# Performance work log

Hardware: AMD Instinct MI355X
Metric: run time of the kernel (lower is better)

The kernel has to match this reference:

```python
import jax, jax.numpy as jnp
import numpy as np

H = 2048   # hidden_size
NH = 32    # n_head
HS = 64    # head_size
B, T = 2, 4096
D_DECAY, D_AAA, D_MV, D_GATE = 96, 96, 64, 256


def setup_inputs() -> dict:
    key = jax.random.key(0)
    ks = jax.random.split(key, 30)
    rn = lambda k, s, sc=0.02: jax.random.normal(k, s, jnp.float32) * sc
    d = {}
    d['x'] = jax.random.normal(ks[0], (B, T, H), jnp.float32)
    d['shift_state_in'] = jax.random.normal(ks[1], (B, H), jnp.float32)
    d['wkv_state_in'] = jnp.zeros((B, NH, HS, HS), jnp.float32)
    d['v_first_val'] = jax.random.normal(ks[2], (B, T, H), jnp.float32)
    for i, n in enumerate(['x_r', 'x_w', 'x_k', 'x_v', 'x_a', 'x_g']):
        d[n] = jax.random.uniform(ks[3 + i], (H,), jnp.float32)
    d['w0'] = rn(ks[9], (H,)) - 4.0
    d['w1'] = rn(ks[10], (H, D_DECAY)); d['w2'] = rn(ks[11], (D_DECAY, H))
    d['a0'] = rn(ks[12], (H,)); d['a1'] = rn(ks[13], (H, D_AAA)); d['a2'] = rn(ks[14], (D_AAA, H))
    d['v0'] = rn(ks[15], (H,)) + 1.0; d['v1'] = rn(ks[16], (H, D_MV)); d['v2'] = rn(ks[17], (D_MV, H))
    d['g1'] = rn(ks[18], (H, D_GATE)); d['g2'] = rn(ks[19], (D_GATE, H))
    d['k_k'] = jnp.full((H,), 0.85, jnp.float32)
    d['k_a'] = jnp.ones((H,), jnp.float32)
    d['r_k'] = rn(ks[20], (NH, HS))
    s = 1.0 / np.sqrt(H)
    d['W_r'] = jax.random.normal(ks[21], (H, H), jnp.float32) * s
    d['W_k'] = jax.random.normal(ks[22], (H, H), jnp.float32) * s
    d['W_v'] = jax.random.normal(ks[23], (H, H), jnp.float32) * s
    d['W_o'] = jax.random.normal(ks[24], (H, H), jnp.float32) * s
    d['ln_w'] = jnp.ones((H,), jnp.float32)
    d['ln_b'] = jnp.zeros((H,), jnp.float32)
    return d


def _forward(x, shift_state_in, wkv_state_in, v_first_val, x_r, x_w, x_k, x_v, x_a, x_g,
             w0, w1, w2, a0, a1, a2, v0, v1, v2, g1, g2, k_k, k_a, r_k,
             W_r, W_k, W_v, W_o, ln_w, ln_b):
    Bx, Tx, C = x.shape
    # token shift: previous token embedding (shift_state for t=0)
    xprev = jnp.concatenate([shift_state_in[:, None, :], x[:, :-1]], axis=1)
    dx = xprev - x
    xr, xw, xk, xv, xa, xg = (x + dx * m for m in (x_r, x_w, x_k, x_v, x_a, x_g))
    r = xr @ W_r.T
    k = xk @ W_k.T
    v = xv @ W_v.T
    # soft-clamped log-decay (<= -0.5)
    w_raw = -jax.nn.softplus(-(w0 + jnp.tanh(xw @ w1) @ w2)) - 0.5
    # layer_id > 0: residual mix with first-layer value
    v = v + (v_first_val - v) * jax.nn.sigmoid(v0 + (xv @ v1) @ v2)
    a = jax.nn.sigmoid(a0 + (xa @ a1) @ a2)          # in-context learning rate
    g = jax.nn.sigmoid(xg @ g1) @ g2                 # output gate
    kk = (k * k_k).reshape(Bx, Tx, NH, HS)
    kk = kk / jnp.maximum(jnp.linalg.norm(kk, axis=-1, keepdims=True), 1e-12)  # F.normalize
    kk = kk.reshape(Bx, Tx, C)
    k = k * (1.0 + (a - 1.0) * k_a)
    w = jnp.exp(-jnp.exp(w_raw))                     # per-channel decay in (0,1)
    heads = lambda t: t.reshape(Bx, Tx, NH, HS).transpose(1, 0, 2, 3)  # [T,B,NH,HS]
    rs, ws, ks_, vs, kks, as_ = map(heads, (r, w, k, v, kk, a))

    def step(S, inp):
        # S: [B,NH,HS(value),HS(key)]
        rt, wt, kt, vt, kkt, at = inp
        sa = jnp.einsum('bhvk,bhk->bhv', S, -kkt)
        S = (S * wt[:, :, None, :]
             + sa[:, :, :, None] * (kkt * at)[:, :, None, :]
             + vt[:, :, :, None] * kt[:, :, None, :])
        return S, jnp.einsum('bhvk,bhk->bhv', S, rt)

    wkv_state_out, y = jax.lax.scan(step, wkv_state_in, (rs, ws, ks_, vs, kks, as_))
    y = y.transpose(1, 0, 2, 3)                      # [B,T,NH,HS]
    # GroupNorm(n_head groups, eps=1e-5*head_size)
    mu = y.mean(-1, keepdims=True)
    var = y.var(-1, keepdims=True)
    y = ((y - mu) / jnp.sqrt(var + 1e-5 * HS)).reshape(Bx, Tx, C) * ln_w + ln_b
    rk = (r.reshape(Bx, Tx, NH, HS) * k.reshape(Bx, Tx, NH, HS) * r_k).sum(-1, keepdims=True)
    y = y + (rk * v.reshape(Bx, Tx, NH, HS)).reshape(Bx, Tx, C)
    out = (y * g) @ W_o.T
    return out, x[:, -1], wkv_state_out, v_first_val


def reference(x, shift_state_in, wkv_state_in, v_first_val, x_r, x_w, x_k, x_v, x_a, x_g,
              w0, w1, w2, a0, a1, a2, v0, v1, v2, g1, g2, k_k, k_a, r_k,
              W_r, W_k, W_v, W_o, ln_w, ln_b):
    return _forward(x, shift_state_in, wkv_state_in, v_first_val, x_r, x_w, x_k, x_v, x_a, x_g,
                    w0, w1, w2, a0, a1, a2, v0, v1, v2, g1, g2, k_k, k_a, r_k,
                    W_r, W_k, W_v, W_o, ln_w, ln_b)
```

## Files before the change

kernel.cpp:

```cpp
#include <hip/hip_runtime.h>

typedef unsigned short u16;
typedef __attribute__((ext_vector_type(4))) float f32x4;
typedef __attribute__((ext_vector_type(8))) __bf16 bf16x8;
typedef __attribute__((ext_vector_type(8))) unsigned short u16x8;
typedef __attribute__((ext_vector_type(4))) unsigned short u16x4;

#define DI static __device__ __forceinline__

DI float bfu2f(u16 u){ unsigned int x = ((unsigned int)u)<<16; float f; __builtin_memcpy(&f,&x,4); return f; }
DI u16 f2bfu(float f){ __bf16 h = (__bf16)f; u16 u; __builtin_memcpy(&u,&h,2); return u; }
DI float sigm(float x){ return 1.f/(1.f+expf(-x)); }

DI void gload_lds16(const void* g, void* l) {
  __builtin_amdgcn_global_load_lds(
      (const __attribute__((address_space(1))) unsigned int*)g,
      (__attribute__((address_space(3))) unsigned int*)l, 16, 0, 0);
}

template<bool OBF16>
__global__ __launch_bounds__(256) void gemm128_k(
    const u16* __restrict__ A, const u16* __restrict__ Bt,
    void* __restrict__ Cp, int M, int N, int K)
{
  __shared__ alignas(16) u16 As[128*64];
  __shared__ alignas(16) u16 Bs[128*64];
  const int tid = threadIdx.x;
  const int wid = tid >> 6, lane = tid & 63;
  const int wm = wid >> 1, wn = wid & 1;
  const int l15 = lane & 15, q = lane >> 4;
  const int m0 = blockIdx.x * 128, n0 = blockIdx.y * 128;
  const int sr = (wid << 3) + (lane >> 3);
  const int sc = (lane & 7) << 3;
  f32x4 acc[4][4];
  #pragma unroll
  for (int i=0;i<4;i++)
    #pragma unroll
    for (int j=0;j<4;j++) acc[i][j] = f32x4{0.f,0.f,0.f,0.f};

  char* la = (char*)As + (size_t)wid*1024;
  char* lb = (char*)Bs + (size_t)wid*1024;
  for (int k0 = 0; k0 < K; k0 += 64) {
    const u16* ga = A  + (size_t)(m0 + sr)*K + k0 + sc;
    const u16* gb = Bt + (size_t)(n0 + sr)*K + k0 + sc;
    #pragma unroll
    for (int it = 0; it < 4; ++it) {
      gload_lds16(ga + (size_t)(32*it)*K, la + it*4096);
      gload_lds16(gb + (size_t)(32*it)*K, lb + it*4096);
    }
    __syncthreads();
    #pragma unroll
    for (int ks = 0; ks < 64; ks += 32) {
      bf16x8 af[4], bfv[4];
      #pragma unroll
      for (int i=0;i<4;i++) af[i]  = *(const bf16x8*)&As[(wm*64 + i*16 + l15)*64 + ks + q*8];
      #pragma unroll
      for (int j=0;j<4;j++) bfv[j] = *(const bf16x8*)&Bs[(wn*64 + j*16 + l15)*64 + ks + q*8];
      #pragma unroll
      for (int i=0;i<4;i++)
        #pragma unroll
        for (int j=0;j<4;j++)
          acc[i][j] = __builtin_amdgcn_mfma_f32_16x16x32_bf16(af[i], bfv[j], acc[i][j], 0, 0, 0);
    }
    __syncthreads();
  }
  #pragma unroll
  for (int i=0;i<4;i++)
    #pragma unroll
    for (int j=0;j<4;j++)
      #pragma unroll
      for (int rr=0;rr<4;rr++) {
        const int gm = m0 + wm*64 + i*16 + q*4 + rr;
        const int gn = n0 + wn*64 + j*16 + l15;
        const size_t o = (size_t)gm * (size_t)N + gn;
        if constexpr (OBF16) ((u16*)Cp)[o] = f2bfu(acc[i][j][rr]);
        else                 ((float*)Cp)[o] = acc[i][j][rr];
      }
}

constexpr int LDW = 72;

template<bool MIX, bool WNK, bool ABF16, bool OBF16, int EPI=0>
__global__ __launch_bounds__(256) void gemm_k(
    const void* __restrict__ Ap, const float* __restrict__ dxp, const float* __restrict__ mixp,
    const float* __restrict__ Wp, void* __restrict__ Cp, int M, int N, int K)
{
  __shared__ alignas(16) __bf16 As[64*LDW];
  __shared__ alignas(16) __bf16 Bs[64*LDW];
  const int tid = threadIdx.x;
  const int m0 = blockIdx.x * 64;
  const int n0 = blockIdx.y * 64;
  const int lane = tid & 63, wid = tid >> 6;
  const int wm = wid >> 1, wn = wid & 1;
  const int l15 = lane & 15, q = lane >> 4;
  f32x4 acc[2][2] = {{{0.f,0.f,0.f,0.f},{0.f,0.f,0.f,0.f}},
                     {{0.f,0.f,0.f,0.f},{0.f,0.f,0.f,0.f}}};

  for (int k0 = 0; k0 < K; k0 += 64) {
    {
      const int kc = (tid & 7) * 8;
      const int r0 = tid >> 3;
      #pragma unroll
      for (int it = 0; it < 2; ++it) {
        const int row = r0 + 32*it;
        const size_t gmK = (size_t)(m0 + row) * (size_t)K;
        const int gk = k0 + kc;
        if constexpr (ABF16) {
          const u16* A16 = (const u16*)Ap;
          u16x8 u;
          if (gk + 7 < K) u = *(const u16x8*)(A16 + gmK + gk);
          else {
            #pragma unroll
            for (int e=0;e<8;e++) u[e] = (gk+e < K) ? A16[gmK + gk + e] : (u16)0;
          }
          *(u16x8*)&As[row*LDW + kc] = u;
        } else {
          const float* A32 = (const float*)Ap;
          float f[8];
          if (gk + 7 < K) {
            f32x4 va = *(const f32x4*)(A32 + gmK + gk);
            f32x4 vb = *(const f32x4*)(A32 + gmK + gk + 4);
            if constexpr (MIX) {
              f32x4 d0 = *(const f32x4*)(dxp + gmK + gk);
              f32x4 d1 = *(const f32x4*)(dxp + gmK + gk + 4);
              f32x4 c0 = *(const f32x4*)(mixp + gk);
              f32x4 c1 = *(const f32x4*)(mixp + gk + 4);
              va = va + d0*c0; vb = vb + d1*c1;
            }
            #pragma unroll
            for (int e=0;e<4;e++){ f[e]=va[e]; f[4+e]=vb[e]; }
          } else {
            #pragma unroll
            for (int e=0;e<8;e++){
              const int kk2 = gk+e;
              float xv = 0.f;
              if (kk2 < K) {
                xv = A32[gmK + kk2];
                if constexpr (MIX) xv = fmaf(dxp[gmK+kk2], mixp[kk2], xv);
              }
              f[e] = xv;
            }
          }
          bf16x8 v8;
          #pragma unroll
          for (int e=0;e<8;e++) v8[e] = (__bf16)f[e];
          *(bf16x8*)&As[row*LDW + kc] = v8;
        }
      }
    }
    if constexpr (WNK) {
      const int kc = (tid & 7) * 8;
      const int r0 = tid >> 3;
      #pragma unroll
      for (int it = 0; it < 2; ++it) {
        const int row = r0 + 32*it;
        const int gn = n0 + row;
        const int gk = k0 + kc;
        float f[8];
        if (gn < N && gk + 7 < K) {
          const size_t o = (size_t)gn * (size_t)K + gk;
          f32x4 va = *(const f32x4*)(Wp + o);
          f32x4 vb = *(const f32x4*)(Wp + o + 4);
          #pragma unroll
          for (int e=0;e<4;e++){ f[e]=va[e]; f[4+e]=vb[e]; }
        } else {
          #pragma unroll
          for (int e=0;e<8;e++) f[e] = (gn < N && gk+e < K) ? Wp[(size_t)gn*K + gk + e] : 0.f;
        }
        bf16x8 v8;
        #pragma unroll
        for (int e=0;e<8;e++) v8[e] = (__bf16)f[e];
        *(bf16x8*)&Bs[row*LDW + kc] = v8;
      }
    } else {
      const int nc = (tid & 15) * 4;
      const int kr = tid >> 4;
      #pragma unroll
      for (int it = 0; it < 4; ++it) {
        const int kk = kr + 16*it;
        const int gk = k0 + kk;
        f32x4 v = {0.f,0.f,0.f,0.f};
        if (gk < K) {
          const int gn = n0 + nc;
          if (gn + 3 < N) v = *(const f32x4*)(Wp + (size_t)gk*N + gn);
          else {
            #pragma unroll
            for (int e=0;e<4;e++) if (gn+e < N) v[e] = Wp[(size_t)gk*N + gn + e];
          }
        }
        #pragma unroll
        for (int e=0;e<4;e++) Bs[(nc+e)*LDW + kk] = (__bf16)v[e];
      }
    }
    __syncthreads();
    #pragma unroll
    for (int ks = 0; ks < 64; ks += 32) {
      bf16x8 af[2], bfv[2];
      #pragma unroll
      for (int i=0;i<2;i++) af[i]  = *(const bf16x8*)&As[(wm*32 + i*16 + l15)*LDW + ks + q*8];
      #pragma unroll
      for (int i=0;i<2;i++) bfv[i] = *(const bf16x8*)&Bs[(wn*32 + i*16 + l15)*LDW + ks + q*8];
      #pragma unroll
      for (int i=0;i<2;i++)
        #pragma unroll
        for (int j=0;j<2;j++)
          acc[i][j] = __builtin_amdgcn_mfma_f32_16x16x32_bf16(af[i], bfv[j], acc[i][j], 0, 0, 0);
    }
    __syncthreads();
  }
  #pragma unroll
  for (int i=0;i<2;i++) {
    #pragma unroll
    for (int j=0;j<2;j++) {
      #pragma unroll
      for (int rr=0;rr<4;rr++) {
        const int gm = m0 + wm*32 + i*16 + q*4 + rr;
        const int gn = n0 + wn*32 + j*16 + l15;
        if (gn < N) {
          const size_t o = (size_t)gm * (size_t)N + gn;
          if constexpr (EPI == 1) {
            float* C = (float*)Cp;
            const float s = sigm(mixp[gn] + acc[i][j][rr]);
            const float vG = C[o];
            C[o] = vG + (dxp[o] - vG) * s;
          } else if constexpr (OBF16) {
            ((u16*)Cp)[o] = f2bfu(acc[i][j][rr]);
          } else {
            ((float*)Cp)[o] = acc[i][j][rr];
          }
        }
      }
    }
  }
}

__global__ void mix_cast_k(const float* __restrict__ x, const float* __restrict__ shift,
    const float* __restrict__ mr, const float* __restrict__ mw, const float* __restrict__ mk,
    const float* __restrict__ mv, const float* __restrict__ ma, const float* __restrict__ mg,
    u16* __restrict__ xr_b, u16* __restrict__ xw_b, u16* __restrict__ xk_b,
    u16* __restrict__ xv_b, u16* __restrict__ xa_b, u16* __restrict__ xg_b,
    float* __restrict__ xlast, int T_, int B_)
{
  const int Hh = 2048;
  size_t e4 = (size_t)blockIdx.x*blockDim.x + threadIdx.x;
  size_t total4 = (size_t)B_*T_*Hh/4;
  if (e4 >= total4) return;
  size_t e = e4*4;
  size_t th = (size_t)T_*Hh;
  size_t b = e / th; size_t rem = e - b*th;
  int t = (int)(rem / Hh); int c = (int)(rem & (Hh-1));
  f32x4 xv4 = *(const f32x4*)(x+e);
  f32x4 xp = t ? *(const f32x4*)(x+e-Hh) : *(const f32x4*)(shift + b*Hh + c);
  f32x4 dx = xp - xv4;
  if (t == T_-1) *(f32x4*)(xlast + b*Hh + c) = xv4;
  #define EMIT(mp, dst) { \
    f32x4 mc = *(const f32x4*)(mp + c); \
    f32x4 r_ = xv4 + dx*mc; \
    u16x4 o_; \
    o_[0]=f2bfu(r_[0]); o_[1]=f2bfu(r_[1]); o_[2]=f2bfu(r_[2]); o_[3]=f2bfu(r_[3]); \
    *(u16x4*)(dst + e) = o_; }
  EMIT(mr, xr_b) EMIT(mw, xw_b) EMIT(mk, xk_b)
  EMIT(mv, xv_b) EMIT(ma, xa_b) EMIT(mg, xg_b)
  #undef EMIT
}

__global__ void castw_k(const float* __restrict__ src, u16* __restrict__ dst, long n4){
  long i = (long)blockIdx.x*blockDim.x + threadIdx.x;
  if (i < n4) {
    f32x4 v = ((const f32x4*)src)[i];
    u16x4 o; o[0]=f2bfu(v[0]); o[1]=f2bfu(v[1]); o[2]=f2bfu(v[2]); o[3]=f2bfu(v[3]);
    ((u16x4*)dst)[i] = o;
  }
}

__global__ void ew_tanh_k(u16* p, long n){
  long i = (long)blockIdx.x*blockDim.x + threadIdx.x;
  if (i < n) p[i] = f2bfu(tanhf(bfu2f(p[i])));
}
__global__ void ew_sig_k(u16* p, long n){
  long i = (long)blockIdx.x*blockDim.x + threadIdx.x;
  if (i < n) p[i] = f2bfu(sigm(bfu2f(p[i])));
}
__global__ void ew_w_k(float* p, const float* __restrict__ w0, long n){
  long i = (long)blockIdx.x*blockDim.x + threadIdx.x;
  if (i < n) {
    int c = (int)(i & 2047);
    float z = -(w0[c] + p[i]);
    float sp = (z > 20.f) ? z : log1pf(expf(z));
    p[i] = expf(-expf(-sp - 0.5f));
  }
}
__global__ void ew_a_k(u16* p, const float* __restrict__ a0, long n){
  long i = (long)blockIdx.x*blockDim.x + threadIdx.x;
  if (i < n) { int c = (int)(i & 2047); p[i] = f2bfu(sigm(a0[c] + bfu2f(p[i]))); }
}
__global__ void copy4_k(float* __restrict__ dst, const float* __restrict__ src, long n4){
  long i = (long)blockIdx.x*blockDim.x + threadIdx.x;
  if (i < n4) ((f32x4*)dst)[i] = ((const f32x4*)src)[i];
}

__global__ __launch_bounds__(256) void rnorm_k(
    const u16* __restrict__ kb, const float* __restrict__ kkw, float* __restrict__ r2)
{
  const size_t bt = blockIdx.x;
  const int tid = threadIdx.x;
  const int c0 = tid << 3;
  u16x8 kv8 = *(const u16x8*)(kb + bt*2048 + c0);
  f32x4 ka_ = *(const f32x4*)(kkw + c0);
  f32x4 kb_ = *(const f32x4*)(kkw + c0 + 4);
  float s = 0.f;
  #pragma unroll
  for (int e=0;e<4;e++){ float kk = bfu2f(kv8[e])*ka_[e];   s = fmaf(kk,kk,s); }
  #pragma unroll
  for (int e=0;e<4;e++){ float kk = bfu2f(kv8[4+e])*kb_[e]; s = fmaf(kk,kk,s); }
  s += __shfl_xor(s, 1, 64);
  s += __shfl_xor(s, 2, 64);
  s += __shfl_xor(s, 4, 64);
  if ((tid & 7) == 0) r2[bt*32 + (tid>>3)] = 1.f/fmaxf(s, 1e-24f);
}

__global__ __launch_bounds__(64) __attribute__((amdgpu_waves_per_eu(1, 4)))
void scan_k(
    const u16* __restrict__ rb, const float* __restrict__ wb, const u16* __restrict__ kb,
    const float* __restrict__ vb, const u16* __restrict__ ab,
    const float* __restrict__ kkw, const float* __restrict__ kaw,
    const float* __restrict__ S0, float* __restrict__ yb, float* __restrict__ Sout, int T_)
{
  const int Hh = 2048, NHl = 32;
  const int blk = blockIdx.x;
  const int b = blk >> 5, h = blk & 31;
  const int lane = threadIdx.x;
  float S[64];
  const size_t sbase = (((size_t)b*NHl + h)*64 + lane)*64;
  #pragma unroll
  for (int i=0;i<64;i++) S[i] = S0[sbase+i];
  const float kkc = kkw[h*64+lane], kac = kaw[h*64+lane];
  __shared__ alignas(16) float lw[64], lkk[64], lka[64], lke[64], lr[64];
  size_t idx = (size_t)b*T_*Hh + (size_t)h*64 + lane;
  float rv = bfu2f(rb[idx]), wv = wb[idx], kv = bfu2f(kb[idx]), vv = vb[idx], av = bfu2f(ab[idx]);
  for (int t=0; t<T_; ++t) {
    float kk = kv * kkc;
    float ssum = kk*kk;
    #pragma unroll
    for (int m=1;m<64;m<<=1) ssum += __shfl_xor(ssum, m, 64);
    float inv = 1.f / fmaxf(sqrtf(ssum), 1e-12f);
    float kkn = kk * inv;
    float ke  = kv * (1.f + (av - 1.f)*kac);
    lw[lane]=wv; lkk[lane]=kkn; lka[lane]=kkn*av; lke[lane]=ke; lr[lane]=rv;
    const float vt = vv;
    __syncthreads();
    float nrv=0.f,nwv=0.f,nkv=0.f,nvv=0.f,nav=0.f;
    if (t+1 < T_) {
      const size_t ni = idx + Hh;
      nrv = bfu2f(rb[ni]); nwv = wb[ni]; nkv = bfu2f(kb[ni]); nvv = vb[ni]; nav = bfu2f(ab[ni]);
    }
    const f32x4* KK4 = (const f32x4*)lkk;
    const f32x4* W4  = (const f32x4*)lw;
    const f32x4* KA4 = (const f32x4*)lka;
    const f32x4* KE4 = (const f32x4*)lke;
    const f32x4* R4  = (const f32x4*)lr;
    float sa0=0.f,sa1=0.f,sa2=0.f,sa3=0.f;
    #pragma unroll
    for (int qq=0;qq<16;qq++){
      f32x4 k4 = KK4[qq];
      sa0 = fmaf(S[4*qq+0], k4[0], sa0);
      sa1 = fmaf(S[4*qq+1], k4[1], sa1);
      sa2 = fmaf(S[4*qq+2], k4[2], sa2);
      sa3 = fmaf(S[4*qq+3], k4[3], sa3);
    }
    const float sa = -((sa0+sa1)+(sa2+sa3));
    float y0=0.f,y1=0.f,y2=0.f,y3=0.f;
    #pragma unroll
    for (int qq=0;qq<16;qq++){
      f32x4 w4=W4[qq], a4=KA4[qq], e4=KE4[qq], r4=R4[qq];
      float s_;
      s_ = fmaf(vt, e4[0], fmaf(sa, a4[0], S[4*qq+0]*w4[0])); S[4*qq+0]=s_; y0 = fmaf(s_, r4[0], y0);
      s_ = fmaf(vt, e4[1], fmaf(sa, a4[1], S[4*qq+1]*w4[1])); S[4*qq+1]=s_; y1 = fmaf(s_, r4[1], y1);
      s_ = fmaf(vt, e4[2], fmaf(sa, a4[2], S[4*qq+2]*w4[2])); S[4*qq+2]=s_; y2 = fmaf(s_, r4[2], y2);
      s_ = fmaf(vt, e4[3], fmaf(sa, a4[3], S[4*qq+3]*w4[3])); S[4*qq+3]=s_; y3 = fmaf(s_, r4[3], y3);
    }
    yb[idx] = (y0+y1)+(y2+y3);
    __syncthreads();
    rv=nrv; wv=nwv; kv=nkv; vv=nvv; av=nav;
    idx += Hh;
  }
  #pragma unroll
  for (int i=0;i<64;i++) Sout[sbase+i] = S[i];
}

__global__ __launch_bounds__(64) void chunk_mu_k(
    const float* __restrict__ wb, const u16* __restrict__ kb,
    const float* __restrict__ vb, const u16* __restrict__ ab,
    const float* __restrict__ kkw, const float* __restrict__ kaw,
    const float* __restrict__ r2b,
    float* __restrict__ Mbuf, float* __restrict__ Ubuf, int T_, int NC)
{
  const int bid = blockIdx.x;
  const int ch  = bid >> 1;
  const bool idrow = ((bid & 1) == 0);
  const int c  = ch % NC;
  const int bh = ch / NC;
  const int b = bh >> 5, h = bh & 31;
  const int lane = threadIdx.x;

  float S[64];
  #pragma unroll
  for (int i=0;i<64;i++) S[i] = (idrow && lane == i) ? 1.f : 0.f;

  const int hc = h*64 + lane;
  const float kkc = kkw[hc], kac = kaw[hc];

  __shared__ alignas(16) float LB[2][4][64];

  size_t idx = ((size_t)b*T_ + (size_t)c*64)*2048 + hc;
  size_t r2i = ((size_t)b*T_ + (size_t)c*64)*32 + h;

  {
    const float kv = bfu2f(kb[idx]);
    const float av = bfu2f(ab[idx]);
    const float kk = kv*kkc;
    LB[0][0][lane] = wb[idx];
    LB[0][1][lane] = kk;
    LB[0][2][lane] = kk*av;
    if (!idrow) LB[0][3][lane] = kv*(1.f+(av-1.f)*kac);
  }
  float vv = idrow ? 0.f : vb[idx];
  float r2 = r2b[r2i];
  __syncthreads();

  for (int j=0; j<64; ++j) {
    const int cur = j & 1;
    float nk=0.f,nw=0.f,na=0.f,nv=0.f,nr2=0.f;
    if (j+1 < 64) {
      const size_t ni = idx + 2048;
      nk = bfu2f(kb[ni]); nw = wb[ni]; na = bfu2f(ab[ni]);
      if (!idrow) nv = vb[ni];
      nr2 = r2b[r2i + 32];
    }
    const f32x4* W4  = (const f32x4*)LB[cur][0];
    const f32x4* KK4 = (const f32x4*)LB[cur][1];
    const f32x4* KA4 = (const f32x4*)LB[cur][2];
    const f32x4* KE4 = (const f32x4*)LB[cur][3];
    float sa0=0.f,sa1=0.f,sa2=0.f,sa3=0.f;
    #pragma unroll
    for (int qq=0;qq<16;qq++){
      f32x4 k4 = KK4[qq];
      sa0 = fmaf(S[4*qq+0], k4[0], sa0);
      sa1 = fmaf(S[4*qq+1], k4[1], sa1);
      sa2 = fmaf(S[4*qq+2], k4[2], sa2);
      sa3 = fmaf(S[4*qq+3], k4[3], sa3);
    }
    const float sa = -((sa0+sa1)+(sa2+sa3)) * r2;
    const float vtv = vv;
    if (idrow) {
      #pragma unroll
      for (int qq=0;qq<16;qq++){
        f32x4 w4=W4[qq], a4=KA4[qq];
        S[4*qq+0] = fmaf(sa, a4[0], S[4*qq+0]*w4[0]);
        S[4*qq+1] = fmaf(sa, a4[1], S[4*qq+1]*w4[1]);
        S[4*qq+2] = fmaf(sa, a4[2], S[4*qq+2]*w4[2]);
        S[4*qq+3] = fmaf(sa, a4[3], S[4*qq+3]*w4[3]);
      }
    } else {
      #pragma unroll
      for (int qq=0;qq<16;qq++){
        f32x4 w4=W4[qq], a4=KA4[qq], e4=KE4[qq];
        S[4*qq+0] = fmaf(vtv, e4[0], fmaf(sa, a4[0], S[4*qq+0]*w4[0]));
        S[4*qq+1] = fmaf(vtv, e4[1], fmaf(sa, a4[1], S[4*qq+1]*w4[1]));
        S[4*qq+2] = fmaf(vtv, e4[2], fmaf(sa, a4[2], S[4*qq+2]*w4[2]));
        S[4*qq+3] = fmaf(vtv, e4[3], fmaf(sa, a4[3], S[4*qq+3]*w4[3]));
      }
    }
    if (j+1 < 64) {
      const float kk = nk*kkc;
      LB[cur^1][0][lane] = nw;
      LB[cur^1][1][lane] = kk;
      LB[cur^1][2][lane] = kk*na;
      if (!idrow) LB[cur^1][3][lane] = nk*(1.f+(na-1.f)*kac);
    }
    __syncthreads();
    vv = nv; r2 = nr2;
    idx += 2048; r2i += 32;
  }
  float* dst = (idrow ? Mbuf : Ubuf) + (size_t)ch*4096 + (size_t)lane*64;
  #pragma unroll
  for (int qq=0;qq<16;qq++)
    *(f32x4*)(dst + 4*qq) = f32x4{S[4*qq+0],S[4*qq+1],S[4*qq+2],S[4*qq+3]};
}

__global__ __launch_bounds__(256) void propagate_k(
    const float* __restrict__ Mbuf, const float* __restrict__ Ubuf,
    const float* __restrict__ S0, float* __restrict__ SSbuf, float* __restrict__ Sout, int NC)
{
  const int bh   = blockIdx.x >> 2;
  const int v0r  = (blockIdx.x & 3) * 16;
  const int tid  = threadIdx.x;
  const int lane = tid & 63;
  const int wvv  = tid >> 6;

  __shared__ float MT[64*65];
  __shared__ float Srow[16][64];

  #pragma unroll
  for (int i=0;i<4;i++) {
    const int v = v0r + wvv*4 + i;
    Srow[wvv*4+i][lane] = S0[((size_t)bh*64 + v)*64 + lane];
  }

  const size_t mbase = (size_t)bh * NC * 4096;
  f32x4 mreg[4];
  #pragma unroll
  for (int it=0; it<4; ++it)
    mreg[it] = *(const f32x4*)(Mbuf + mbase + it*1024 + tid*4);

  for (int c=0; c<NC; ++c) {
    const size_t chB = mbase + (size_t)c*4096;
    #pragma unroll
    for (int it=0; it<4; ++it) {
      const int base = it*1024 + tid*4;
      const int j = base >> 6;
      const int k = base & 63;
      #pragma unroll
      for (int e=0;e<4;e++) MT[(k+e)*65 + j] = mreg[it][e];
    }
    __syncthreads();
    if (c+1 < NC) {
      #pragma unroll
      for (int it=0; it<4; ++it)
        mreg[it] = *(const f32x4*)(Mbuf + chB + 4096 + it*1024 + tid*4);
    }
    #pragma unroll
    for (int i=0;i<4;i++)
      SSbuf[chB + (size_t)(v0r + wvv*4 + i)*64 + lane] = Srow[wvv*4+i][lane];
    float u[4];
    #pragma unroll
    for (int i=0;i<4;i++)
      u[i] = Ubuf[chB + (size_t)(v0r + wvv*4 + i)*64 + lane];
    float acc[4] = {0.f,0.f,0.f,0.f};
    #pragma unroll
    for (int j4=0; j4<16; ++j4) {
      float m0_ = MT[lane*65 + j4*4 + 0];
      float m1_ = MT[lane*65 + j4*4 + 1];
      float m2_ = MT[lane*65 + j4*4 + 2];
      float m3_ = MT[lane*65 + j4*4 + 3];
      #pragma unroll
      for (int i=0;i<4;i++) {
        f32x4 s4 = *(const f32x4*)&Srow[wvv*4+i][j4*4];
        acc[i] = fmaf(s4[0], m0_, acc[i]);
        acc[i] = fmaf(s4[1], m1_, acc[i]);
        acc[i] = fmaf(s4[2], m2_, acc[i]);
        acc[i] = fmaf(s4[3], m3_, acc[i]);
      }
    }
    #pragma unroll
    for (int i=0;i<4;i++) Srow[wvv*4+i][lane] = acc[i] + u[i];
    __syncthreads();
  }
  #pragma unroll
  for (int i=0;i<4;i++) {
    const int v = v0r + wvv*4 + i;
    Sout[((size_t)bh*64 + v)*64 + lane] = Srow[wvv*4+i][lane];
  }
}

__global__ __launch_bounds__(64) void replay_k(
    const u16* __restrict__ rb, const float* __restrict__ wb, const u16* __restrict__ kb,
    const float* __restrict__ vb, const u16* __restrict__ ab,
    const float* __restrict__ kkw, const float* __restrict__ kaw,
    const float* __restrict__ r2b,
    const float* __restrict__ SSbuf, float* __restrict__ yb, int T_, int NC)
{
  const int ch = blockIdx.x;
  const int c  = ch % NC;
  const int bh = ch / NC;
  const int b = bh >> 5, h = bh & 31;
  const int lane = threadIdx.x;
  float S[64];
  const float* sp = SSbuf + (size_t)ch*4096 + (size_t)lane*64;
  #pragma unroll
  for (int qq=0;qq<16;qq++){
    f32x4 v4 = *(const f32x4*)(sp + 4*qq);
    S[4*qq+0]=v4[0]; S[4*qq+1]=v4[1]; S[4*qq+2]=v4[2]; S[4*qq+3]=v4[3];
  }
  const int hc = h*64 + lane;
  const float kkc = kkw[hc], kac = kaw[hc];
  __shared__ alignas(16) float LB[2][5][64];
  size_t idx = ((size_t)b*T_ + (size_t)c*64)*2048 + hc;
  size_t r2i = ((size_t)b*T_ + (size_t)c*64)*32 + h;
  {
    const float kv = bfu2f(kb[idx]);
    const float av = bfu2f(ab[idx]);
    const float kk = kv*kkc;
    LB[0][0][lane] = wb[idx];
    LB[0][1][lane] = kk;
    LB[0][2][lane] = kk*av;
    LB[0][3][lane] = kv*(1.f+(av-1.f)*kac);
    LB[0][4][lane] = bfu2f(rb[idx]);
  }
  float vv = vb[idx];
  float r2 = r2b[r2i];
  __syncthreads();

  for (int t=0; t<64; ++t) {
    const int cur = t & 1;
    float nr=0.f,nw=0.f,nk=0.f,nv=0.f,na=0.f,nr2=0.f;
    if (t+1 < 64) {
      const size_t ni = idx + 2048;
      nr = bfu2f(rb[ni]); nw = wb[ni]; nk = bfu2f(kb[ni]); nv = vb[ni]; na = bfu2f(ab[ni]);
      nr2 = r2b[r2i + 32];
    }
    const f32x4* W4  = (const f32x4*)LB[cur][0];
    const f32x4* KK4 = (const f32x4*)LB[cur][1];
    const f32x4* KA4 = (const f32x4*)LB[cur][2];
    const f32x4* KE4 = (const f32x4*)LB[cur][3];
    const f32x4* R4  = (const f32x4*)LB[cur][4];
    float sa0=0.f,sa1=0.f,sa2=0.f,sa3=0.f;
    #pragma unroll
    for (int qq=0;qq<16;qq++){
      f32x4 k4 = KK4[qq];
      sa0 = fmaf(S[4*qq+0], k4[0], sa0);
      sa1 = fmaf(S[4*qq+1], k4[1], sa1);
      sa2 = fmaf(S[4*qq+2], k4[2], sa2);
      sa3 = fmaf(S[4*qq+3], k4[3], sa3);
    }
    const float sa = -((sa0+sa1)+(sa2+sa3)) * r2;
    const float vt = vv;
    float y0=0.f,y1=0.f,y2=0.f,y3=0.f;
    #pragma unroll
    for (int qq=0;qq<16;qq++){
      f32x4 w4=W4[qq], a4=KA4[qq], e4=KE4[qq], r4=R4[qq];
      float s_;
      s_ = fmaf(vt, e4[0], fmaf(sa, a4[0], S[4*qq+0]*w4[0])); S[4*qq+0]=s_; y0 = fmaf(s_, r4[0], y0);
      s_ = fmaf(vt, e4[1], fmaf(sa, a4[1], S[4*qq+1]*w4[1])); S[4*qq+1]=s_; y1 = fmaf(s_, r4[1], y1);
      s_ = fmaf(vt, e4[2], fmaf(sa, a4[2], S[4*qq+2]*w4[2])); S[4*qq+2]=s_; y2 = fmaf(s_, r4[2], y2);
      s_ = fmaf(vt, e4[3], fmaf(sa, a4[3], S[4*qq+3]*w4[3])); S[4*qq+3]=s_; y3 = fmaf(s_, r4[3], y3);
    }
    yb[idx] = (y0+y1)+(y2+y3);
    if (t+1 < 64) {
      const float kk = nk*kkc;
      LB[cur^1][0][lane] = nw;
      LB[cur^1][1][lane] = kk;
      LB[cur^1][2][lane] = kk*na;
      LB[cur^1][3][lane] = nk*(1.f+(na-1.f)*kac);
      LB[cur^1][4][lane] = nr;
    }
    __syncthreads();
    vv = nv; r2 = nr2;
    idx += 2048; r2i += 32;
  }
}

__global__ __launch_bounds__(256) void post_k(
    const float* __restrict__ yb, const u16* __restrict__ rb, const u16* __restrict__ kb,
    const u16* __restrict__ ab, const u16* __restrict__ gb, const float* __restrict__ vb,
    const float* __restrict__ kaw, const float* __restrict__ rkw,
    const float* __restrict__ lnw, const float* __restrict__ lnb, u16* __restrict__ zb)
{
  const int wid = threadIdx.x >> 6, lane = threadIdx.x & 63;
  const size_t unit = (size_t)blockIdx.x*4 + wid;
  const size_t bt = unit >> 5; const int h = (int)(unit & 31);
  const size_t idx = bt*2048 + (size_t)h*64 + lane;
  const int hc = h*64 + lane;
  const float yv = yb[idx];
  const float rv = bfu2f(rb[idx]), kv = bfu2f(kb[idx]), av = bfu2f(ab[idx]);
  const float ke = kv*(1.f + (av-1.f)*kaw[hc]);
  float s1 = yv, s2 = yv*yv, rk = rv*ke*rkw[hc];
  #pragma unroll
  for (int m=1;m<64;m<<=1){
    s1 += __shfl_xor(s1,m,64);
    s2 += __shfl_xor(s2,m,64);
    rk += __shfl_xor(rk,m,64);
  }
  const float mean = s1 * (1.f/64.f);
  const float var  = s2 * (1.f/64.f) - mean*mean;
  const float rstd = rsqrtf(var + 6.4e-4f);
  const float zn = (yv-mean)*rstd*lnw[hc] + lnb[hc] + rk*vb[idx];
  zb[idx] = f2bfu(zn * bfu2f(gb[idx]));
}

extern "C" void kernel_launch(void* const* d_in, const int* in_sizes, int n_in,
                              void* d_out, int out_size, void* d_ws, size_t ws_size,
                              hipStream_t stream)
{
  const float* x      = (const float*)d_in[0];
  const float* shift  = (const float*)d_in[1];
  const float* wkv0   = (const float*)d_in[2];
  const float* vfirst = (const float*)d_in[3];
  const float* xr = (const float*)d_in[4];
  const float* xw = (const float*)d_in[5];
  const float* xk = (const float*)d_in[6];
  const float* xv = (const float*)d_in[7];
  const float* xa = (const float*)d_in[8];
  const float* xg = (const float*)d_in[9];
  const float* w0 = (const float*)d_in[10];
  const float* w1 = (const float*)d_in[11];
  const float* w2 = (const float*)d_in[12];
  const float* a0 = (const float*)d_in[13];
  const float* a1 = (const float*)d_in[14];
  const float* a2 = (const float*)d_in[15];
  const float* v0 = (const float*)d_in[16];
  const float* v1 = (const float*)d_in[17];
  const float* v2 = (const float*)d_in[18];
  const float* g1 = (const float*)d_in[19];
  const float* g2 = (const float*)d_in[20];
  const float* k_k = (const float*)d_in[21];
  const float* k_a = (const float*)d_in[22];
  const float* r_k = (const float*)d_in[23];
  const float* W_r = (const float*)d_in[24];
  const float* W_k = (const float*)d_in[25];
  const float* W_v = (const float*)d_in[26];
  const float* W_o = (const float*)d_in[27];
  const float* ln_w = (const float*)d_in[28];
  const float* ln_b = (const float*)d_in[29];

  const int H = 2048, NH = 32;
  const int BH = in_sizes[1];
  const int B  = BH / H;
  const long BTH = (long)in_sizes[0];
  const int T  = (int)(BTH / BH);
  const int M  = (int)(BTH / H);

  float* out0 = (float*)d_out;
  float* out1 = out0 + BTH;
  float* out2 = out1 + BH;
  float* out3 = out2 + (size_t)B*NH*64*64;

  char* ws = (char*)d_ws;
  u16* mixb = (u16*)ws;  ws += (size_t)BTH*12;
  u16* xr_b = mixb + 0*BTH;
  u16* xw_b = mixb + 1*BTH;
  u16* xk_b = mixb + 2*BTH;
  u16* xv_b = mixb + 3*BTH;
  u16* xa_b = mixb + 4*BTH;
  u16* xg_b = mixb + 5*BTH;
  float* Mbuf  = (float*)mixb;
  float* Ubuf  = Mbuf + BTH;
  float* SSbuf = Ubuf + BTH;
  u16*   zb16  = (u16*)mixb;
  u16* rb   = (u16*)ws;  ws += BTH*2;
  u16* kb   = (u16*)ws;  ws += BTH*2;
  u16* ab   = (u16*)ws;  ws += BTH*2;
  u16* gb   = (u16*)ws;  ws += BTH*2;
  u16* wr16 = (u16*)ws;  ws += (size_t)H*H*2;
  u16* wk16 = (u16*)ws;  ws += (size_t)H*H*2;
  u16* wv16 = (u16*)ws;  ws += (size_t)H*H*2;
  u16* wo16 = (u16*)ws;  ws += (size_t)H*H*2;
  u16* h1w  = (u16*)ws;  ws += (size_t)M*96*2;
  u16* h1a  = (u16*)ws;  ws += (size_t)M*96*2;
  u16* h1v  = (u16*)ws;  ws += (size_t)M*64*2;
  u16* h1g  = (u16*)ws;  ws += (size_t)M*256*2;
  float* dxz = (float*)ws; ws += BTH*4;
  float* r2b = (float*)h1w;
  const size_t ws_need = (size_t)(ws - (char*)d_ws);
  const bool chunked = (ws_size >= ws_need) && (T % 64 == 0);
  const bool big_ok  = (M % 128 == 0);
  (void)n_in; (void)out_size;

  const dim3 blk(256);
  auto gg  = [&](int N){ return dim3(M/64, (N+63)/64); };
  auto gg128 = [&](int N){ return dim3(M/128, N/128); };

  mix_cast_k<<<dim3((unsigned)((BTH/4 + 255)/256)), blk, 0, stream>>>(
      x, shift, xr, xw, xk, xv, xa, xg, xr_b, xw_b, xk_b, xv_b, xa_b, xg_b, out1, T, B);

  {
    const long n4 = (long)H*H/4;
    const dim3 gw((unsigned)((n4 + 255)/256));
    castw_k<<<gw, blk, 0, stream>>>(W_r, wr16, n4);
    castw_k<<<gw, blk, 0, stream>>>(W_k, wk16, n4);
    castw_k<<<gw, blk, 0, stream>>>(W_v, wv16, n4);
    castw_k<<<gw, blk, 0, stream>>>(W_o, wo16, n4);
  }

  gemm_k<false,false,true,true><<<gg(96),  blk, 0, stream>>>(xw_b, nullptr, nullptr, w1, h1w, M, 96,  H);
  gemm_k<false,false,true,true><<<gg(96),  blk, 0, stream>>>(xa_b, nullptr, nullptr, a1, h1a, M, 96,  H);
  gemm_k<false,false,true,true><<<gg(64),  blk, 0, stream>>>(xv_b, nullptr, nullptr, v1, h1v, M, 64,  H);
  gemm_k<false,false,true,true><<<gg(256), blk, 0, stream>>>(xg_b, nullptr, nullptr, g1, h1g, M, 256, H);

  ew_tanh_k<<<dim3((unsigned)(((long)M*96 + 255)/256)),  blk, 0, stream>>>(h1w, (long)M*96);
  ew_sig_k <<<dim3((unsigned)(((long)M*256 + 255)/256)), blk, 0, stream>>>(h1g, (long)M*256);

  if (big_ok) {
    gemm128_k<true ><<<gg128(H), blk, 0, stream>>>(xr_b, wr16, rb,   M, H, H);
    gemm128_k<true ><<<gg128(H), blk, 0, stream>>>(xk_b, wk16, kb,   M, H, H);
    gemm128_k<false><<<gg128(H), blk, 0, stream>>>(xv_b, wv16, out3, M, H, H);
  } else {
    gemm_k<false,true,true,true ><<<gg(H), blk, 0, stream>>>(xr_b, nullptr, nullptr, W_r, rb,   M, H, H);
    gemm_k<false,true,true,true ><<<gg(H), blk, 0, stream>>>(xk_b, nullptr, nullptr, W_k, kb,   M, H, H);
    gemm_k<false,true,true,false><<<gg(H), blk, 0, stream>>>(xv_b, nullptr, nullptr, W_v, out3, M, H, H);
  }

  gemm_k<false,false,true,false  ><<<gg(H), blk, 0, stream>>>(h1w, nullptr, nullptr, w2, dxz, M, H, 96);
  rnorm_k<<<dim3((unsigned)M), blk, 0, stream>>>(kb, k_k, r2b);
  gemm_k<false,false,true,true   ><<<gg(H), blk, 0, stream>>>(h1a, nullptr, nullptr, a2, ab,  M, H, 96);
  gemm_k<false,false,true,false,1><<<gg(H), blk, 0, stream>>>(h1v, vfirst,  v0,      v2, out3, M, H, 64);
  gemm_k<false,false,true,true   ><<<gg(H), blk, 0, stream>>>(h1g, nullptr, nullptr, g2, gb,  M, H, 256);

  const unsigned nbB = (unsigned)((BTH + 255)/256);
  ew_w_k<<<dim3(nbB), blk, 0, stream>>>(dxz, w0, BTH);
  ew_a_k<<<dim3(nbB), blk, 0, stream>>>(ab, a0, BTH);

  if (chunked) {
    const int NC = T / 64;
    const int CH = B * NH * NC;
    chunk_mu_k <<<dim3(2*CH),   dim3(64),  0, stream>>>(dxz, kb, out3, ab, k_k, k_a, r2b, Mbuf, Ubuf, T, NC);
    propagate_k<<<dim3(B*NH*4), blk,       0, stream>>>(Mbuf, Ubuf, wkv0, SSbuf, out2, NC);
    replay_k   <<<dim3(CH),     dim3(64),  0, stream>>>(rb, dxz, kb, out3, ab, k_k, k_a, r2b, SSbuf, out0, T, NC);
  } else {
    scan_k<<<dim3(B*NH), dim3(64), 0, stream>>>(rb, dxz, kb, out3, ab, k_k, k_a, wkv0, out0, out2, T);
  }

  post_k<<<dim3((unsigned)((size_t)M*NH/4)), blk, 0, stream>>>(out0, rb, kb, ab, gb, out3,
                                                               k_a, r_k, ln_w, ln_b, zb16);

  copy4_k<<<dim3((unsigned)((BTH/4 + 255)/256)), blk, 0, stream>>>(out3, vfirst, BTH/4);

  if (big_ok) {
    gemm128_k<false><<<gg128(H), blk, 0, stream>>>(zb16, wo16, out0, M, H, H);
  } else {
    gemm_k<false,true,true,false><<<gg(H), blk, 0, stream>>>(zb16, nullptr, nullptr, W_o, out0, M, H, H);
  }
}
```

Before: 1.989 ms.

## Fuse chunk transition and zero-state replay, add low-rank output correction

The chunked WKV scan now runs one pass per chunk that evolves the identity-started transition matrix and the zero-start update together. It also emits the zero-start outputs and a per-step decay projection D (the transition applied to r). After propagating the chunk start states, a new lightweight kernel adds the correction S_start·D to each output instead of replaying the full recurrence. This removes the separate replay pass and its recompute of the state recurrence, at the cost of twice the register state per thread (128 floats) and an extra 64x64 buffer per chunk. SSbuf is aliased onto Ubuf, which is overwritten in place during propagation.

```diff
diff --git a/kernel.cpp b/kernel.cpp
--- a/kernel.cpp
+++ b/kernel.cpp
@@ -389,204 +389,32 @@
 }
 
 __global__ __launch_bounds__(64) void chunk_mu_k(
-    const float* __restrict__ wb, const u16* __restrict__ kb,
-    const float* __restrict__ vb, const u16* __restrict__ ab,
-    const float* __restrict__ kkw, const float* __restrict__ kaw,
-    const float* __restrict__ r2b,
-    float* __restrict__ Mbuf, float* __restrict__ Ubuf, int T_, int NC)
-{
-  const int bid = blockIdx.x;
-  const int ch  = bid >> 1;
-  const bool idrow = ((bid & 1) == 0);
-  const int c  = ch % NC;
-  const int bh = ch / NC;
-  const int b = bh >> 5, h = bh & 31;
-  const int lane = threadIdx.x;
-
-  float S[64];
-  #pragma unroll
-  for (int i=0;i<64;i++) S[i] = (idrow && lane == i) ? 1.f : 0.f;
-
-  const int hc = h*64 + lane;
-  const float kkc = kkw[hc], kac = kaw[hc];
-
-  __shared__ alignas(16) float LB[2][4][64];
-
-  size_t idx = ((size_t)b*T_ + (size_t)c*64)*2048 + hc;
-  size_t r2i = ((size_t)b*T_ + (size_t)c*64)*32 + h;
-
-  {
-    const float kv = bfu2f(kb[idx]);
-    const float av = bfu2f(ab[idx]);
-    const float kk = kv*kkc;
-    LB[0][0][lane] = wb[idx];
-    LB[0][1][lane] = kk;
-    LB[0][2][lane] = kk*av;
-    if (!idrow) LB[0][3][lane] = kv*(1.f+(av-1.f)*kac);
-  }
-  float vv = idrow ? 0.f : vb[idx];
-  float r2 = r2b[r2i];
-  __syncthreads();
-
-  for (int j=0; j<64; ++j) {
-    const int cur = j & 1;
-    float nk=0.f,nw=0.f,na=0.f,nv=0.f,nr2=0.f;
-    if (j+1 < 64) {
-      const size_t ni = idx + 2048;
-      nk = bfu2f(kb[ni]); nw = wb[ni]; na = bfu2f(ab[ni]);
-      if (!idrow) nv = vb[ni];
-      nr2 = r2b[r2i + 32];
-    }
-    const f32x4* W4  = (const f32x4*)LB[cur][0];
-    const f32x4* KK4 = (const f32x4*)LB[cur][1];
-    const f32x4* KA4 = (const f32x4*)LB[cur][2];
-    const f32x4* KE4 = (const f32x4*)LB[cur][3];
-    float sa0=0.f,sa1=0.f,sa2=0.f,sa3=0.f;
-    #pragma unroll
-    for (int qq=0;qq<16;qq++){
-      f32x4 k4 = KK4[qq];
-      sa0 = fmaf(S[4*qq+0], k4[0], sa0);
-      sa1 = fmaf(S[4*qq+1], k4[1], sa1);
-      sa2 = fmaf(S[4*qq+2], k4[2], sa2);
-      sa3 = fmaf(S[4*qq+3], k4[3], sa3);
-    }
-    const float sa = -((sa0+sa1)+(sa2+sa3)) * r2;
-    const float vtv = vv;
-    if (idrow) {
-      #pragma unroll
-      for (int qq=0;qq<16;qq++){
-        f32x4 w4=W4[qq], a4=KA4[qq];
-        S[4*qq+0] = fmaf(sa, a4[0], S[4*qq+0]*w4[0]);
-        S[4*qq+1] = fmaf(sa, a4[1], S[4*qq+1]*w4[1]);
-        S[4*qq+2] = fmaf(sa, a4[2], S[4*qq+2]*w4[2]);
-        S[4*qq+3] = fmaf(sa, a4[3], S[4*qq+3]*w4[3]);
-      }
-    } else {
-      #pragma unroll
-      for (int qq=0;qq<16;qq++){
-        f32x4 w4=W4[qq], a4=KA4[qq], e4=KE4[qq];
-        S[4*qq+0] = fmaf(vtv, e4[0], fmaf(sa, a4[0], S[4*qq+0]*w4[0]));
-        S[4*qq+1] = fmaf(vtv, e4[1], fmaf(sa, a4[1], S[4*qq+1]*w4[1]));
-        S[4*qq+2] = fmaf(vtv, e4[2], fmaf(sa, a4[2], S[4*qq+2]*w4[2]));
-        S[4*qq+3] = fmaf(vtv, e4[3], fmaf(sa, a4[3], S[4*qq+3]*w4[3]));
-      }
-    }
-    if (j+1 < 64) {
-      const float kk = nk*kkc;
-      LB[cur^1][0][lane] = nw;
-      LB[cur^1][1][lane] = kk;
-      LB[cur^1][2][lane] = kk*na;
-      if (!idrow) LB[cur^1][3][lane] = nk*(1.f+(na-1.f)*kac);
-    }
-    __syncthreads();
-    vv = nv; r2 = nr2;
-    idx += 2048; r2i += 32;
-  }
-  float* dst = (idrow ? Mbuf : Ubuf) + (size_t)ch*4096 + (size_t)lane*64;
-  #pragma unroll
-  for (int qq=0;qq<16;qq++)
-    *(f32x4*)(dst + 4*qq) = f32x4{S[4*qq+0],S[4*qq+1],S[4*qq+2],S[4*qq+3]};
-}
-
-__global__ __launch_bounds__(256) void propagate_k(
-    const float* __restrict__ Mbuf, const float* __restrict__ Ubuf,
-    const float* __restrict__ S0, float* __restrict__ SSbuf, float* __restrict__ Sout, int NC)
-{
-  const int bh   = blockIdx.x >> 2;
-  const int v0r  = (blockIdx.x & 3) * 16;
-  const int tid  = threadIdx.x;
-  const int lane = tid & 63;
-  const int wvv  = tid >> 6;
-
-  __shared__ float MT[64*65];
-  __shared__ float Srow[16][64];
-
-  #pragma unroll
-  for (int i=0;i<4;i++) {
-    const int v = v0r + wvv*4 + i;
-    Srow[wvv*4+i][lane] = S0[((size_t)bh*64 + v)*64 + lane];
-  }
-
-  const size_t mbase = (size_t)bh * NC * 4096;
-  f32x4 mreg[4];
-  #pragma unroll
-  for (int it=0; it<4; ++it)
-    mreg[it] = *(const f32x4*)(Mbuf + mbase + it*1024 + tid*4);
-
-  for (int c=0; c<NC; ++c) {
-    const size_t chB = mbase + (size_t)c*4096;
-    #pragma unroll
-    for (int it=0; it<4; ++it) {
-      const int base = it*1024 + tid*4;
-      const int j = base >> 6;
-      const int k = base & 63;
-      #pragma unroll
-      for (int e=0;e<4;e++) MT[(k+e)*65 + j] = mreg[it][e];
-    }
-    __syncthreads();
-    if (c+1 < NC) {
-      #pragma unroll
-      for (int it=0; it<4; ++it)
-        mreg[it] = *(const f32x4*)(Mbuf + chB + 4096 + it*1024 + tid*4);
-    }
-    #pragma unroll
-    for (int i=0;i<4;i++)
-      SSbuf[chB + (size_t)(v0r + wvv*4 + i)*64 + lane] = Srow[wvv*4+i][lane];
-    float u[4];
-    #pragma unroll
-    for (int i=0;i<4;i++)
-      u[i] = Ubuf[chB + (size_t)(v0r + wvv*4 + i)*64 + lane];
-    float acc[4] = {0.f,0.f,0.f,0.f};
-    #pragma unroll
-    for (int j4=0; j4<16; ++j4) {
-      float m0_ = MT[lane*65 + j4*4 + 0];
-      float m1_ = MT[lane*65 + j4*4 + 1];
-      float m2_ = MT[lane*65 + j4*4 + 2];
-      float m3_ = MT[lane*65 + j4*4 + 3];
-      #pragma unroll
-      for (int i=0;i<4;i++) {
-        f32x4 s4 = *(const f32x4*)&Srow[wvv*4+i][j4*4];
-        acc[i] = fmaf(s4[0], m0_, acc[i]);
-        acc[i] = fmaf(s4[1], m1_, acc[i]);
-        acc[i] = fmaf(s4[2], m2_, acc[i]);
-        acc[i] = fmaf(s4[3], m3_, acc[i]);
-      }
-    }
-    #pragma unroll
-    for (int i=0;i<4;i++) Srow[wvv*4+i][lane] = acc[i] + u[i];
-    __syncthreads();
-  }
-  #pragma unroll
-  for (int i=0;i<4;i++) {
-    const int v = v0r + wvv*4 + i;
-    Sout[((size_t)bh*64 + v)*64 + lane] = Srow[wvv*4+i][lane];
-  }
-}
-
-__global__ __launch_bounds__(64) void replay_k(
     const u16* __restrict__ rb, const float* __restrict__ wb, const u16* __restrict__ kb,
     const float* __restrict__ vb, const u16* __restrict__ ab,
     const float* __restrict__ kkw, const float* __restrict__ kaw,
     const float* __restrict__ r2b,
-    const float* __restrict__ SSbuf, float* __restrict__ yb, int T_, int NC)
+    float* __restrict__ Mbuf, float* __restrict__ Ubuf, float* __restrict__ Dbuf,
+    float* __restrict__ yb, int T_, int NC)
 {
   const int ch = blockIdx.x;
   const int c  = ch % NC;
   const int bh = ch / NC;
   const int b = bh >> 5, h = bh & 31;
   const int lane = threadIdx.x;
-  float S[64];
-  const float* sp = SSbuf + (size_t)ch*4096 + (size_t)lane*64;
-  #pragma unroll
-  for (int qq=0;qq<16;qq++){
-    f32x4 v4 = *(const f32x4*)(sp + 4*qq);
-    S[4*qq+0]=v4[0]; S[4*qq+1]=v4[1]; S[4*qq+2]=v4[2]; S[4*qq+3]=v4[3];
-  }
+
+  float SM[64], SU[64];
+  #pragma unroll
+  for (int i=0;i<64;i++) { SM[i] = (lane == i) ? 1.f : 0.f; SU[i] = 0.f; }
+
   const int hc = h*64 + lane;
   const float kkc = kkw[hc], kac = kaw[hc];
+
   __shared__ alignas(16) float LB[2][5][64];
+
   size_t idx = ((size_t)b*T_ + (size_t)c*64)*2048 + hc;
   size_t r2i = ((size_t)b*T_ + (size_t)c*64)*32 + h;
+  float* dD = Dbuf + (size_t)ch*4096 + lane;
+
   {
     const float kv = bfu2f(kb[idx]);
     const float av = bfu2f(ab[idx]);
@@ -601,12 +429,12 @@
   float r2 = r2b[r2i];
   __syncthreads();
 
-  for (int t=0; t<64; ++t) {
-    const int cur = t & 1;
-    float nr=0.f,nw=0.f,nk=0.f,nv=0.f,na=0.f,nr2=0.f;
-    if (t+1 < 64) {
+  for (int j=0; j<64; ++j) {
+    const int cur = j & 1;
+    float nr=0.f,nk=0.f,nw=0.f,na=0.f,nv=0.f,nr2=0.f;
+    if (j+1 < 64) {
       const size_t ni = idx + 2048;
-      nr = bfu2f(rb[ni]); nw = wb[ni]; nk = bfu2f(kb[ni]); nv = vb[ni]; na = bfu2f(ab[ni]);
+      nr = bfu2f(rb[ni]); nk = bfu2f(kb[ni]); nw = wb[ni]; na = bfu2f(ab[ni]); nv = vb[ni];
       nr2 = r2b[r2i + 32];
     }
     const f32x4* W4  = (const f32x4*)LB[cur][0];
@@ -614,29 +442,41 @@
     const f32x4* KA4 = (const f32x4*)LB[cur][2];
     const f32x4* KE4 = (const f32x4*)LB[cur][3];
     const f32x4* R4  = (const f32x4*)LB[cur][4];
-    float sa0=0.f,sa1=0.f,sa2=0.f,sa3=0.f;
+    float m0=0.f,m1=0.f,m2=0.f,m3=0.f;
+    float u0=0.f,u1=0.f,u2=0.f,u3=0.f;
     #pragma unroll
     for (int qq=0;qq<16;qq++){
       f32x4 k4 = KK4[qq];
-      sa0 = fmaf(S[4*qq+0], k4[0], sa0);
-      sa1 = fmaf(S[4*qq+1], k4[1], sa1);
-      sa2 = fmaf(S[4*qq+2], k4[2], sa2);
-      sa3 = fmaf(S[4*qq+3], k4[3], sa3);
-    }
-    const float sa = -((sa0+sa1)+(sa2+sa3)) * r2;
+      m0 = fmaf(SM[4*qq+0], k4[0], m0);
+      m1 = fmaf(SM[4*qq+1], k4[1], m1);
+      m2 = fmaf(SM[4*qq+2], k4[2], m2);
+      m3 = fmaf(SM[4*qq+3], k4[3], m3);
+      u0 = fmaf(SU[4*qq+0], k4[0], u0);
+      u1 = fmaf(SU[4*qq+1], k4[1], u1);
+      u2 = fmaf(SU[4*qq+2], k4[2], u2);
+      u3 = fmaf(SU[4*qq+3], k4[3], u3);
+    }
+    const float saM = -((m0+m1)+(m2+m3)) * r2;
+    const float saU = -((u0+u1)+(u2+u3)) * r2;
     const float vt = vv;
+    float d0=0.f,d1=0.f,d2=0.f,d3=0.f;
     float y0=0.f,y1=0.f,y2=0.f,y3=0.f;
     #pragma unroll
     for (int qq=0;qq<16;qq++){
       f32x4 w4=W4[qq], a4=KA4[qq], e4=KE4[qq], r4=R4[qq];
       float s_;
-      s_ = fmaf(vt, e4[0], fmaf(sa, a4[0], S[4*qq+0]*w4[0])); S[4*qq+0]=s_; y0 = fmaf(s_, r4[0], y0);
-      s_ = fmaf(vt, e4[1], fmaf(sa, a4[1], S[4*qq+1]*w4[1])); S[4*qq+1]=s_; y1 = fmaf(s_, r4[1], y1);
-      s_ = fmaf(vt, e4[2], fmaf(sa, a4[2], S[4*qq+2]*w4[2])); S[4*qq+2]=s_; y2 = fmaf(s_, r4[2], y2);
-      s_ = fmaf(vt, e4[3], fmaf(sa, a4[3], S[4*qq+3]*w4[3])); S[4*qq+3]=s_; y3 = fmaf(s_, r4[3], y3);
-    }
+      s_ = fmaf(saM, a4[0], SM[4*qq+0]*w4[0]); SM[4*qq+0]=s_; d0 = fmaf(s_, r4[0], d0);
+      s_ = fmaf(saM, a4[1], SM[4*qq+1]*w4[1]); SM[4*qq+1]=s_; d1 = fmaf(s_, r4[1], d1);
+      s_ = fmaf(saM, a4[2], SM[4*qq+2]*w4[2]); SM[4*qq+2]=s_; d2 = fmaf(s_, r4[2], d2);
+      s_ = fmaf(saM, a4[3], SM[4*qq+3]*w4[3]); SM[4*qq+3]=s_; d3 = fmaf(s_, r4[3], d3);
+      s_ = fmaf(vt, e4[0], fmaf(saU, a4[0], SU[4*qq+0]*w4[0])); SU[4*qq+0]=s_; y0 = fmaf(s_, r4[0], y0);
+      s_ = fmaf(vt, e4[1], fmaf(saU, a4[1], SU[4*qq+1]*w4[1])); SU[4*qq+1]=s_; y1 = fmaf(s_, r4[1], y1);
+      s_ = fmaf(vt, e4[2], fmaf(saU, a4[2], SU[4*qq+2]*w4[2])); SU[4*qq+2]=s_; y2 = fmaf(s_, r4[2], y2);
+      s_ = fmaf(vt, e4[3], fmaf(saU, a4[3], SU[4*qq+3]*w4[3])); SU[4*qq+3]=s_; y3 = fmaf(s_, r4[3], y3);
+    }
+    dD[(size_t)j*64] = (d0+d1)+(d2+d3);
     yb[idx] = (y0+y1)+(y2+y3);
-    if (t+1 < 64) {
+    if (j+1 < 64) {
       const float kk = nk*kkc;
       LB[cur^1][0][lane] = nw;
       LB[cur^1][1][lane] = kk;
@@ -647,6 +487,145 @@
     __syncthreads();
     vv = nv; r2 = nr2;
     idx += 2048; r2i += 32;
+  }
+  float* md = Mbuf + (size_t)ch*4096 + (size_t)lane*64;
+  float* ud = Ubuf + (size_t)ch*4096 + (size_t)lane*64;
+  #pragma unroll
+  for (int qq=0;qq<16;qq++){
+    *(f32x4*)(md + 4*qq) = f32x4{SM[4*qq+0],SM[4*qq+1],SM[4*qq+2],SM[4*qq+3]};
+    *(f32x4*)(ud + 4*qq) = f32x4{SU[4*qq+0],SU[4*qq+1],SU[4*qq+2],SU[4*qq+3]};
+  }
+}
+
+__global__ __launch_bounds__(256) void propagate_k(
+    const float* __restrict__ Mbuf, const float* Ubuf,
+    const float* __restrict__ S0, float* SSbuf, float* __restrict__ Sout, int NC)
+{
+  const int bh   = blockIdx.x >> 2;
+  const int v0r  = (blockIdx.x & 3) * 16;
+  const int tid  = threadIdx.x;
+  const int lane = tid & 63;
+  const int wvv  = tid >> 6;
+
+  __shared__ float MT[64*65];
+  __shared__ float Srow[16][64];
+
+  #pragma unroll
+  for (int i=0;i<4;i++) {
+    const int v = v0r + wvv*4 + i;
+    Srow[wvv*4+i][lane] = S0[((size_t)bh*64 + v)*64 + lane];
+  }
+
+  const size_t mbase = (size_t)bh * NC * 4096;
+  f32x4 mreg[4];
+  #pragma unroll
+  for (int it=0; it<4; ++it)
+    mreg[it] = *(const f32x4*)(Mbuf + mbase + it*1024 + tid*4);
+
+  for (int c=0; c<NC; ++c) {
+    const size_t chB = mbase + (size_t)c*4096;
+    #pragma unroll
+    for (int it=0; it<4; ++it) {
+      const int base = it*1024 + tid*4;
+      const int j = base >> 6;
+      const int k = base & 63;
+      #pragma unroll
+      for (int e=0;e<4;e++) MT[(k+e)*65 + j] = mreg[it][e];
+    }
+    __syncthreads();
+    if (c+1 < NC) {
+      #pragma unroll
+      for (int it=0; it<4; ++it)
+        mreg[it] = *(const f32x4*)(Mbuf + chB + 4096 + it*1024 + tid*4);
+    }
+    float u[4];
+    #pragma unroll
+    for (int i=0;i<4;i++)
+      u[i] = Ubuf[chB + (size_t)(v0r + wvv*4 + i)*64 + lane];
+    #pragma unroll
+    for (int i=0;i<4;i++)
+      SSbuf[chB + (size_t)(v0r + wvv*4 + i)*64 + lane] = Srow[wvv*4+i][lane];
+    float acc[4] = {0.f,0.f,0.f,0.f};
+    #pragma unroll
+    for (int j4=0; j4<16; ++j4) {
+      float m0_ = MT[lane*65 + j4*4 + 0];
+      float m1_ = MT[lane*65 + j4*4 + 1];
+      float m2_ = MT[lane*65 + j4*4 + 2];
+      float m3_ = MT[lane*65 + j4*4 + 3];
+      #pragma unroll
+      for (int i=0;i<4;i++) {
+        f32x4 s4 = *(const f32x4*)&Srow[wvv*4+i][j4*4];
+        acc[i] = fmaf(s4[0], m0_, acc[i]);
+        acc[i] = fmaf(s4[1], m1_, acc[i]);
+        acc[i] = fmaf(s4[2], m2_, acc[i]);
+        acc[i] = fmaf(s4[3], m3_, acc[i]);
+      }
+    }
+    #pragma unroll
+    for (int i=0;i<4;i++) Srow[wvv*4+i][lane] = acc[i] + u[i];
+    __syncthreads();
+  }
+  #pragma unroll
+  for (int i=0;i<4;i++) {
+    const int v = v0r + wvv*4 + i;
+    Sout[((size_t)bh*64 + v)*64 + lane] = Srow[wvv*4+i][lane];
+  }
+}
+
+__global__ __launch_bounds__(64) void ycorr_k(
+    const float* __restrict__ SSbuf, const float* __restrict__ Dbuf,
+    float* __restrict__ yb, int T_, int NC)
+{
+  const int ch = blockIdx.x;
+  const int c  = ch % NC;
+  const int bh = ch / NC;
+  const int b = bh >> 5, h = bh & 31;
+  const int lane = threadIdx.x;
+
+  __shared__ alignas(16) float Dl[64*68];
+
+  {
+    const float* sg = SSbuf + (size_t)ch*4096;
+    #pragma unroll
+    for (int i=0;i<16;i++){
+      const int o = i*256 + lane*4;
+      f32x4 v = *(const f32x4*)(sg + o);
+      *(f32x4*)&Dl[(o>>6)*68 + (o&63)] = v;
+    }
+  }
+  __syncthreads();
+  float ss[64];
+  #pragma unroll
+  for (int qq=0;qq<16;qq++){
+    f32x4 v = *(const f32x4*)&Dl[lane*68 + 4*qq];
+    ss[4*qq+0]=v[0]; ss[4*qq+1]=v[1]; ss[4*qq+2]=v[2]; ss[4*qq+3]=v[3];
+  }
+  __syncthreads();
+  {
+    const float* dg = Dbuf + (size_t)ch*4096;
+    #pragma unroll
+    for (int i=0;i<16;i++){
+      const int o = i*256 + lane*4;
+      f32x4 v = *(const f32x4*)(dg + o);
+      *(f32x4*)&Dl[(o>>6)*68 + (o&63)] = v;
+    }
+  }
+  __syncthreads();
+
+  size_t idx = ((size_t)b*T_ + (size_t)c*64)*2048 + (size_t)h*64 + lane;
+  for (int t=0; t<64; ++t) {
+    const f32x4* D4 = (const f32x4*)&Dl[t*68];
+    float a0=0.f,a1=0.f,a2=0.f,a3=0.f;
+    #pragma unroll
+    for (int qq=0;qq<16;qq++){
+      f32x4 d4 = D4[qq];
+      a0 = fmaf(ss[4*qq+0], d4[0], a0);
+      a1 = fmaf(ss[4*qq+1], d4[1], a1);
+      a2 = fmaf(ss[4*qq+2], d4[2], a2);
+      a3 = fmaf(ss[4*qq+3], d4[3], a3);
+    }
+    yb[idx] = yb[idx] + ((a0+a1)+(a2+a3));
+    idx += 2048;
   }
 }
 
@@ -735,7 +714,8 @@
   u16* xg_b = mixb + 5*BTH;
   float* Mbuf  = (float*)mixb;
   float* Ubuf  = Mbuf + BTH;
-  float* SSbuf = Ubuf + BTH;
+  float* Dbuf  = Ubuf + BTH;
+  float* SSbuf = Ubuf;
   u16*   zb16  = (u16*)mixb;
   u16* rb   = (u16*)ws;  ws += BTH*2;
   u16* kb   = (u16*)ws;  ws += BTH*2;
@@ -803,9 +783,10 @@
   if (chunked) {
     const int NC = T / 64;
     const int CH = B * NH * NC;
-    chunk_mu_k <<<dim3(2*CH),   dim3(64),  0, stream>>>(dxz, kb, out3, ab, k_k, k_a, r2b, Mbuf, Ubuf, T, NC);
+    chunk_mu_k <<<dim3(CH),     dim3(64),  0, stream>>>(rb, dxz, kb, out3, ab, k_k, k_a, r2b,
+                                                        Mbuf, Ubuf, Dbuf, out0, T, NC);
     propagate_k<<<dim3(B*NH*4), blk,       0, stream>>>(Mbuf, Ubuf, wkv0, SSbuf, out2, NC);
-    replay_k   <<<dim3(CH),     dim3(64),  0, stream>>>(rb, dxz, kb, out3, ab, k_k, k_a, r2b, SSbuf, out0, T, NC);
+    ycorr_k    <<<dim3(CH),     dim3(64),  0, stream>>>(SSbuf, Dbuf, out0, T, NC);
   } else {
     scan_k<<<dim3(B*NH), dim3(64), 0, stream>>>(rb, dxz, kb, out3, ab, k_k, k_a, wkv0, out0, out2, T);
   }
```

Measured after the change: 2.209 ms. 11.1% more time.
